# Performance work log

Hardware: AMD Instinct MI355X
Metric: run time of the kernel (lower is better)

## Reference

```python
import jax, jax.numpy as jnp
import numpy as np

N, E, H, C = 50000, 800000, 4, 64
IN_DIM = 128
HID = H * C            # 256, concat output width
VH = C // 2            # 32, value-head hidden
OUT_DIM = 4
NEG_SLOPE = 0.2
LN_EPS = 1e-5


def setup_inputs() -> dict:
    key = jax.random.key(0)
    ks = iter(jax.random.split(key, 64))
    def nrm(shape, s=0.05):
        return jax.random.normal(next(ks), shape, jnp.float32) * s
    inp = {
        "x": jax.random.normal(next(ks), (N, IN_DIM), jnp.float32),
        "edge_src": jax.random.randint(next(ks), (E,), 0, N, dtype=jnp.int32),
        "edge_dst": jax.random.randint(next(ks), (E,), 0, N, dtype=jnp.int32),
        "proj_w": nrm((C, IN_DIM)),
        "proj_b": jnp.zeros((C,), jnp.float32),
    }
    in_dims = [C, HID, HID]
    out_feats = [HID, HID, C]
    for i in range(3):
        inp[f"w{i}"] = nrm((HID, in_dims[i]))
        inp[f"asrc{i}"] = nrm((H, C))
        inp[f"adst{i}"] = nrm((H, C))
        inp[f"b{i}"] = jnp.zeros((out_feats[i],), jnp.float32)
        inp[f"g{i}"] = jnp.ones((out_feats[i],), jnp.float32)
        inp[f"be{i}"] = jnp.zeros((out_feats[i],), jnp.float32)
    inp["vw1"] = nrm((VH, C)); inp["vb1"] = jnp.zeros((VH,), jnp.float32)
    inp["vw2"] = nrm((OUT_DIM, VH)); inp["vb2"] = jnp.zeros((OUT_DIM,), jnp.float32)
    return inp


def _layer_norm(x, g, b):
    mu = x.mean(-1, keepdims=True)
    var = ((x - mu) ** 2).mean(-1, keepdims=True)
    return (x - mu) * jax.lax.rsqrt(var + LN_EPS) * g + b


def _gat_conv(x, src, dst, w, a_s, a_d, bias, concat):
    # x: [N, in_dim] -> h: [N, H, C]
    n = x.shape[0]
    h = (x @ w.T).reshape(n, H, C)
    asrc = jnp.einsum('nhc,hc->nh', h, a_s)  # [N, H]
    adst = jnp.einsum('nhc,hc->nh', h, a_d)
    # PyG default add_self_loops=True
    loop = jnp.arange(n, dtype=src.dtype)
    src_f = jnp.concatenate([src, loop])
    dst_f = jnp.concatenate([dst, loop])
    alpha = jax.nn.leaky_relu(asrc[src_f] + adst[dst_f], NEG_SLOPE)  # [E+N, H]
    # segment softmax over incoming edges of each destination node
    amax = jax.ops.segment_max(alpha, dst_f, num_segments=n)
    ex = jnp.exp(alpha - amax[dst_f])
    denom = jax.ops.segment_sum(ex, dst_f, num_segments=n)
    coef = ex / (denom[dst_f] + 1e-16)
    out = jax.ops.segment_sum(h[src_f] * coef[:, :, None], dst_f, num_segments=n)
    out = out.reshape(n, H * C) if concat else out.mean(axis=1)
    return out + bias


def _gat_layer(x, src, dst, w, a_s, a_d, bias, g, be, concat):
    # GATConv -> LayerNorm -> ELU (dropout is identity in eval)
    return jax.nn.elu(_layer_norm(_gat_conv(x, src, dst, w, a_s, a_d, bias, concat), g, be))


def reference(x, edge_src, edge_dst, proj_w, proj_b,
              w0, asrc0, adst0, b0, g0, be0,
              w1, asrc1, adst1, b1, g1, be1,
              w2, asrc2, adst2, b2, g2, be2,
              vw1, vb1, vw2, vb2):
    h = jax.nn.elu(x @ proj_w.T + proj_b)
    h = _gat_layer(h, edge_src, edge_dst, w0, asrc0, adst0, b0, g0, be0, True)
    h = _gat_layer(h, edge_src, edge_dst, w1, asrc1, adst1, b1, g1, be1, True)
    h = _gat_layer(h, edge_src, edge_dst, w2, asrc2, adst2, b2, g2, be2, False)
    v = jax.nn.elu(h @ vw1.T + vb1)
    return v @ vw2.T + vb2
```

## Files before the change

kernel.cpp:

```cpp
#include <hip/hip_runtime.h>

typedef unsigned short u16;
typedef u16 u16x4 __attribute__((ext_vector_type(4)));
typedef short short8 __attribute__((ext_vector_type(8)));
typedef float f32x4 __attribute__((ext_vector_type(4)));

__device__ __forceinline__ float elu_f(float x) { return x > 0.f ? x : expm1f(x); }
__device__ __forceinline__ float lrelu_f(float x) { return x > 0.f ? x : 0.2f * x; }

__device__ __forceinline__ u16 f2b(float f) {
  union { float f; unsigned u; } v; v.f = f;
  unsigned r = v.u + 0x7FFF + ((v.u >> 16) & 1);
  return (u16)(r >> 16);
}
__device__ __forceinline__ float b2f(u16 u) {
  union { unsigned u; float f; } v; v.u = ((unsigned)u) << 16; return v.f;
}

__global__ __launch_bounds__(256) void cvtdeg_k(const float* __restrict__ x, u16* __restrict__ xb,
                                                int nx8,
                                                const float* __restrict__ pw,
                                                const float* __restrict__ w0,
                                                const float* __restrict__ w1,
                                                const float* __restrict__ w2,
                                                u16* __restrict__ dp, u16* __restrict__ d0,
                                                u16* __restrict__ d1, u16* __restrict__ d2,
                                                const int* __restrict__ edst,
                                                int E, int n, int* __restrict__ deg) {
  int i = blockIdx.x * 256 + threadIdx.x;
  if (i < nx8) {
    int j = i * 8;
    float4 a = *reinterpret_cast<const float4*>(&x[j]);
    float4 b = *reinterpret_cast<const float4*>(&x[j + 4]);
    u16x4 o0, o1;
    o0.x = f2b(a.x); o0.y = f2b(a.y); o0.z = f2b(a.z); o0.w = f2b(a.w);
    o1.x = f2b(b.x); o1.y = f2b(b.y); o1.z = f2b(b.z); o1.w = f2b(b.w);
    *reinterpret_cast<u16x4*>(&xb[j]) = o0;
    *reinterpret_cast<u16x4*>(&xb[j + 4]) = o1;
  } else if (i < nx8 + 155648) {
    int j = i - nx8;
    if (j < 8192) dp[j] = f2b(pw[j]);
    else if (j < 24576) d0[j - 8192] = f2b(w0[j - 8192]);
    else if (j < 90112) d1[j - 24576] = f2b(w1[j - 24576]);
    else d2[j - 90112] = f2b(w2[j - 90112]);
  } else {
    int j = i - (nx8 + 155648);
    if (j < E) atomicAdd(&deg[edst[j]], 1);
    else if (j < E + n) atomicAdd(&deg[j - E], 1);
  }
}

__global__ __launch_bounds__(256) void block_sum_k(const int* __restrict__ deg,
                                                   int* __restrict__ bsum, int n) {
  int i = blockIdx.x * 256 + threadIdx.x;
  int v = (i < n) ? deg[i] : 0;
#pragma unroll
  for (int off = 1; off < 64; off <<= 1) v += __shfl_xor(v, off);
  __shared__ int ws[4];
  if ((threadIdx.x & 63) == 0) ws[threadIdx.x >> 6] = v;
  __syncthreads();
  if (threadIdx.x == 0) bsum[blockIdx.x] = ws[0] + ws[1] + ws[2] + ws[3];
}

__global__ void scan_bsum_k(int* __restrict__ bsum, int nb) {
  __shared__ int s[1024];
  int tid = threadIdx.x;
  int v = (tid < nb) ? bsum[tid] : 0;
  s[tid] = v;
  __syncthreads();
  for (int off = 1; off < 1024; off <<= 1) {
    int t = (tid >= off) ? s[tid - off] : 0;
    __syncthreads();
    s[tid] += t;
    __syncthreads();
  }
  if (tid < nb) bsum[tid] = s[tid] - v;
}

__global__ __launch_bounds__(256) void block_scan_k(const int* __restrict__ deg,
                                                    const int* __restrict__ bsum,
                                                    int* __restrict__ rowptr,
                                                    int* __restrict__ cursor, int n) {
  int i = blockIdx.x * 256 + threadIdx.x;
  int lane = threadIdx.x & 63, w = threadIdx.x >> 6;
  int v = (i < n) ? deg[i] : 0;
  int x = v;
#pragma unroll
  for (int off = 1; off < 64; off <<= 1) {
    int t = __shfl_up(x, off);
    if (lane >= off) x += t;
  }
  __shared__ int ws[4];
  if (lane == 63) ws[w] = x;
  __syncthreads();
  int add = bsum[blockIdx.x];
  for (int j = 0; j < w; ++j) add += ws[j];
  int excl = x - v + add;
  if (i < n) {
    cursor[i] = excl;
    rowptr[i + 1] = excl + v;
  }
  if (i == 0) rowptr[0] = 0;
}

__global__ __launch_bounds__(256) void scatter4_k(const int* __restrict__ src,
                                                  const int* __restrict__ dst,
                                                  int E, int EE, int* __restrict__ cursor,
                                                  int* __restrict__ col, int* __restrict__ dst2) {
  int base = (blockIdx.x * 256 + threadIdx.x) * 4;
  int s[4], d[4], pos[4];
#pragma unroll
  for (int k = 0; k < 4; ++k) {
    int e = base + k;
    if (e < E) { s[k] = src[e]; d[k] = dst[e]; }
    else if (e < EE) { s[k] = d[k] = e - E; }
    else { d[k] = -1; s[k] = 0; }
  }
#pragma unroll
  for (int k = 0; k < 4; ++k)
    if (d[k] >= 0) pos[k] = atomicAdd(&cursor[d[k]], 1);
#pragma unroll
  for (int k = 0; k < 4; ++k)
    if (d[k] >= 0) { col[pos[k]] = s[k]; dst2[pos[k]] = d[k]; }
}

template <int PROJ>
__global__ __launch_bounds__(512) void gemm2_k(const u16* __restrict__ A, int lda,
                                               const u16* __restrict__ W,
                                               const u16* __restrict__ pw,
                                               const float* __restrict__ pb,
                                               u16* __restrict__ Cb,
                                               int n, int K,
                                               const float* __restrict__ a_sv,
                                               const float* __restrict__ a_dv,
                                               float* __restrict__ asrcN,
                                               float* __restrict__ adstN) {
  __shared__ char Asb[128 * 128];
  __shared__ char Bsb[256 * 128];
  __shared__ char Xsb[PROJ ? 128 * 272 : 16];
  __shared__ char Psb[PROJ ? 64 * 272 : 16];
  const int t = threadIdx.x;
  const int lane = t & 63, w = t >> 6;
  const int wrow = w >> 2, wcol = w & 3;
  const int row0 = blockIdx.x * 128;

  if (PROJ) {
#pragma unroll
    for (int i = 0; i < 4; ++i) {
      int ci = i * 512 + t;
      int r = ci >> 4;
      int b = (ci & 15) << 4;
      int ar = row0 + r; ar = ar < n ? ar : n - 1;
      *reinterpret_cast<int4*>(Xsb + r * 272 + b) =
          *reinterpret_cast<const int4*>(&A[(size_t)ar * 128 + (b >> 1)]);
    }
#pragma unroll
    for (int i = 0; i < 2; ++i) {
      int ci = i * 512 + t;
      int r = ci >> 4;
      int b = (ci & 15) << 4;
      *reinterpret_cast<int4*>(Psb + r * 272 + b) =
          *reinterpret_cast<const int4*>(&pw[r * 128 + (b >> 1)]);
    }
    __syncthreads();
    f32x4 pacc[4];
#pragma unroll
    for (int nf = 0; nf < 4; ++nf) pacc[nf] = (f32x4){0.f, 0.f, 0.f, 0.f};
#pragma unroll
    for (int ks = 0; ks < 4; ++ks) {
      short8 paf = *reinterpret_cast<const short8*>(
          Xsb + (w * 16 + (lane & 15)) * 272 + ks * 64 + (lane >> 4) * 16);
#pragma unroll
      for (int nf = 0; nf < 4; ++nf) {
        short8 pbf = *reinterpret_cast<const short8*>(
            Psb + (nf * 16 + (lane & 15)) * 272 + ks * 64 + (lane >> 4) * 16);
        pacc[nf] = __builtin_amdgcn_mfma_f32_16x16x32_bf16(paf, pbf, pacc[nf], 0, 0, 0);
      }
    }
#pragma unroll
    for (int nf = 0; nf < 4; ++nf) {
#pragma unroll
      for (int j = 0; j < 4; ++j) {
        int rl = w * 16 + (lane >> 4) * 4 + j;
        int cg = nf * 16 + (lane & 15);
        u16 bv = f2b(elu_f(pacc[nf][j] + pb[cg]));
        *reinterpret_cast<u16*>(Asb + rl * 128 + ((cg * 2) ^ ((rl & 7) << 4))) = bv;
      }
    }
  }

  f32x4 acc[4][4];
#pragma unroll
  for (int m = 0; m < 4; ++m)
#pragma unroll
    for (int nf = 0; nf < 4; ++nf) acc[m][nf] = (f32x4){0.f, 0.f, 0.f, 0.f};

  for (int k0 = 0; k0 < K; k0 += 64) {
    if (!PROJ) {
#pragma unroll
      for (int i = 0; i < 2; ++i) {
        int ci = i * 512 + t;
        int r = ci >> 3;
        int b = (ci & 7) << 4;
        int sw = b ^ ((r & 7) << 4);
        int ar = row0 + r; ar = ar < n ? ar : n - 1;
        int4 av = *reinterpret_cast<const int4*>(&A[(size_t)ar * lda + k0 + (b >> 1)]);
        *reinterpret_cast<int4*>(Asb + r * 128 + sw) = av;
      }
    }
#pragma unroll
    for (int i = 0; i < 4; ++i) {
      int ci = i * 512 + t;
      int r = ci >> 3;
      int b = (ci & 7) << 4;
      int sw = b ^ ((r & 7) << 4);
      int4 wv = *reinterpret_cast<const int4*>(&W[(size_t)r * K + k0 + (b >> 1)]);
      *reinterpret_cast<int4*>(Bsb + r * 128 + sw) = wv;
    }
    __syncthreads();
#pragma unroll
    for (int ks = 0; ks < 2; ++ks) {
      short8 af[4], bf[4];
      int kb = ks * 64 + ((lane >> 4) << 4);
#pragma unroll
      for (int m = 0; m < 4; ++m) {
        int r = wrow * 64 + m * 16 + (lane & 15);
        af[m] = *reinterpret_cast<const short8*>(Asb + r * 128 + (kb ^ ((r & 7) << 4)));
      }
#pragma unroll
      for (int nf = 0; nf < 4; ++nf) {
        int r = wcol * 64 + nf * 16 + (lane & 15);
        bf[nf] = *reinterpret_cast<const short8*>(Bsb + r * 128 + (kb ^ ((r & 7) << 4)));
      }
#pragma unroll
      for (int m = 0; m < 4; ++m)
#pragma unroll
        for (int nf = 0; nf < 4; ++nf)
          acc[m][nf] = __builtin_amdgcn_mfma_f32_16x16x32_bf16(af[m], bf[nf], acc[m][nf], 0, 0, 0);
    }
    __syncthreads();
  }
#pragma unroll
  for (int m = 0; m < 4; ++m) {
#pragma unroll
    for (int j = 0; j < 4; ++j) {
      int rg = row0 + wrow * 64 + m * 16 + (lane >> 4) * 4 + j;
      if (rg >= n) continue;
#pragma unroll
      for (int nf = 0; nf < 4; ++nf) {
        int cg = wcol * 64 + nf * 16 + (lane & 15);
        Cb[(size_t)rg * 256 + cg] = f2b(acc[m][nf][j]);
      }
    }
  }
  {
    int h = wcol;
    int ch = lane & 15;
    float as_c[4], ad_c[4];
#pragma unroll
    for (int nf = 0; nf < 4; ++nf) {
      as_c[nf] = a_sv[h * 64 + nf * 16 + ch];
      ad_c[nf] = a_dv[h * 64 + nf * 16 + ch];
    }
#pragma unroll
    for (int m = 0; m < 4; ++m) {
#pragma unroll
      for (int j = 0; j < 4; ++j) {
        float ps = 0.f, pd = 0.f;
#pragma unroll
        for (int nf = 0; nf < 4; ++nf) {
          float v = acc[m][nf][j];
          ps += v * as_c[nf];
          pd += v * ad_c[nf];
        }
#pragma unroll
        for (int off = 1; off < 16; off <<= 1) {
          ps += __shfl_xor(ps, off);
          pd += __shfl_xor(pd, off);
        }
        int rg = row0 + wrow * 64 + m * 16 + (lane >> 4) * 4 + j;
        if ((lane & 15) == 0 && rg < n) {
          asrcN[(size_t)rg * 4 + h] = ps;
          adstN[(size_t)rg * 4 + h] = pd;
        }
      }
    }
  }
}

__global__ __launch_bounds__(256) void edge_ex2_k(const int* __restrict__ col,
                                                  const int* __restrict__ dst2,
                                                  const float* __restrict__ asrcN,
                                                  const float* __restrict__ adstN,
                                                  float* __restrict__ exT, int eep, int EE) {
  int e = blockIdx.x * 256 + threadIdx.x;
  if (e >= EE) return;
  int s = col[e], d = dst2[e];
  float4 as = *reinterpret_cast<const float4*>(&asrcN[(size_t)s * 4]);
  float4 ad = *reinterpret_cast<const float4*>(&adstN[(size_t)d * 4]);
  exT[e]            = __expf(lrelu_f(as.x + ad.x));
  exT[eep + e]      = __expf(lrelu_f(as.y + ad.y));
  exT[2 * eep + e]  = __expf(lrelu_f(as.z + ad.z));
  exT[3 * eep + e]  = __expf(lrelu_f(as.w + ad.w));
}

template <int MODE>
__global__ __launch_bounds__(256) void gat_agg4_k(const u16* __restrict__ feat,
                                                  const float* __restrict__ exT, int eep,
                                                  const int* __restrict__ rowptr,
                                                  const int* __restrict__ col,
                                                  const float* __restrict__ bias,
                                                  const float* __restrict__ g,
                                                  const float* __restrict__ be,
                                                  void* __restrict__ out, int n) {
  int wave = threadIdx.x >> 6, lane = threadIdx.x & 63;
  int node = blockIdx.x * 4 + wave;
  if (node >= n) return;
  int h = lane >> 4;
  const float* exh = exT + (size_t)h * eep;
  int s0 = rowptr[node], s1 = rowptr[node + 1];
  float ax = 0.f, ay = 0.f, az = 0.f, aw = 0.f, den = 0.f;
  int e = s0;
  for (; e + 8 <= s1; e += 8) {
    int p0 = col[e + 0], p1 = col[e + 1], p2 = col[e + 2], p3 = col[e + 3];
    int q0 = col[e + 4], q1 = col[e + 5], q2 = col[e + 6], q3 = col[e + 7];
    float u0 = exh[e + 0], u1 = exh[e + 1], u2 = exh[e + 2], u3 = exh[e + 3];
    float v0 = exh[e + 4], v1 = exh[e + 5], v2 = exh[e + 6], v3 = exh[e + 7];
    u16x4 fp0 = *reinterpret_cast<const u16x4*>(&feat[(size_t)p0 * 256 + lane * 4]);
    u16x4 fp1 = *reinterpret_cast<const u16x4*>(&feat[(size_t)p1 * 256 + lane * 4]);
    u16x4 fp2 = *reinterpret_cast<const u16x4*>(&feat[(size_t)p2 * 256 + lane * 4]);
    u16x4 fp3 = *reinterpret_cast<const u16x4*>(&feat[(size_t)p3 * 256 + lane * 4]);
    u16x4 fq0 = *reinterpret_cast<const u16x4*>(&feat[(size_t)q0 * 256 + lane * 4]);
    u16x4 fq1 = *reinterpret_cast<const u16x4*>(&feat[(size_t)q1 * 256 + lane * 4]);
    u16x4 fq2 = *reinterpret_cast<const u16x4*>(&feat[(size_t)q2 * 256 + lane * 4]);
    u16x4 fq3 = *reinterpret_cast<const u16x4*>(&feat[(size_t)q3 * 256 + lane * 4]);
    den += ((u0 + u1) + (u2 + u3)) + ((v0 + v1) + (v2 + v3));
    ax += u0 * b2f(fp0.x) + u1 * b2f(fp1.x) + u2 * b2f(fp2.x) + u3 * b2f(fp3.x);
    ay += u0 * b2f(fp0.y) + u1 * b2f(fp1.y) + u2 * b2f(fp2.y) + u3 * b2f(fp3.y);
    az += u0 * b2f(fp0.z) + u1 * b2f(fp1.z) + u2 * b2f(fp2.z) + u3 * b2f(fp3.z);
    aw += u0 * b2f(fp0.w) + u1 * b2f(fp1.w) + u2 * b2f(fp2.w) + u3 * b2f(fp3.w);
    ax += v0 * b2f(fq0.x) + v1 * b2f(fq1.x) + v2 * b2f(fq2.x) + v3 * b2f(fq3.x);
    ay += v0 * b2f(fq0.y) + v1 * b2f(fq1.y) + v2 * b2f(fq2.y) + v3 * b2f(fq3.y);
    az += v0 * b2f(fq0.z) + v1 * b2f(fq1.z) + v2 * b2f(fq2.z) + v3 * b2f(fq3.z);
    aw += v0 * b2f(fq0.w) + v1 * b2f(fq1.w) + v2 * b2f(fq2.w) + v3 * b2f(fq3.w);
  }
  for (; e + 4 <= s1; e += 4) {
    int p0 = col[e + 0], p1 = col[e + 1], p2 = col[e + 2], p3 = col[e + 3];
    float u0 = exh[e + 0], u1 = exh[e + 1], u2 = exh[e + 2], u3 = exh[e + 3];
    u16x4 fp0 = *reinterpret_cast<const u16x4*>(&feat[(size_t)p0 * 256 + lane * 4]);
    u16x4 fp1 = *reinterpret_cast<const u16x4*>(&feat[(size_t)p1 * 256 + lane * 4]);
    u16x4 fp2 = *reinterpret_cast<const u16x4*>(&feat[(size_t)p2 * 256 + lane * 4]);
    u16x4 fp3 = *reinterpret_cast<const u16x4*>(&feat[(size_t)p3 * 256 + lane * 4]);
    den += (u0 + u1) + (u2 + u3);
    ax += u0 * b2f(fp0.x) + u1 * b2f(fp1.x) + u2 * b2f(fp2.x) + u3 * b2f(fp3.x);
    ay += u0 * b2f(fp0.y) + u1 * b2f(fp1.y) + u2 * b2f(fp2.y) + u3 * b2f(fp3.y);
    az += u0 * b2f(fp0.z) + u1 * b2f(fp1.z) + u2 * b2f(fp2.z) + u3 * b2f(fp3.z);
    aw += u0 * b2f(fp0.w) + u1 * b2f(fp1.w) + u2 * b2f(fp2.w) + u3 * b2f(fp3.w);
  }
  for (; e < s1; ++e) {
    int s = col[e];
    float xv = exh[e];
    den += xv;
    u16x4 f = *reinterpret_cast<const u16x4*>(&feat[(size_t)s * 256 + lane * 4]);
    ax += xv * b2f(f.x); ay += xv * b2f(f.y); az += xv * b2f(f.z); aw += xv * b2f(f.w);
  }
  float inv = 1.f / den;
  ax *= inv; ay *= inv; az *= inv; aw *= inv;

  if (MODE == 0) {
    float4 b4 = *reinterpret_cast<const float4*>(&bias[lane * 4]);
    float vx = ax + b4.x, vy = ay + b4.y, vz = az + b4.z, vw = aw + b4.w;
    float s = vx + vy + vz + vw;
#pragma unroll
    for (int off = 1; off < 64; off <<= 1) s += __shfl_xor(s, off);
    float mu = s * (1.f / 256.f);
    float dx = vx - mu, dy = vy - mu, dz = vz - mu, dw = vw - mu;
    float q = dx * dx + dy * dy + dz * dz + dw * dw;
#pragma unroll
    for (int off = 1; off < 64; off <<= 1) q += __shfl_xor(q, off);
    float inv2 = rsqrtf(q * (1.f / 256.f) + 1e-5f);
    float4 gg = *reinterpret_cast<const float4*>(&g[lane * 4]);
    float4 bb = *reinterpret_cast<const float4*>(&be[lane * 4]);
    u16x4 o;
    o.x = f2b(elu_f(dx * inv2 * gg.x + bb.x));
    o.y = f2b(elu_f(dy * inv2 * gg.y + bb.y));
    o.z = f2b(elu_f(dz * inv2 * gg.z + bb.z));
    o.w = f2b(elu_f(dw * inv2 * gg.w + bb.w));
    u16* rowb = (u16*)out + (size_t)node * 256;
    *reinterpret_cast<u16x4*>(&rowb[lane * 4]) = o;
  } else {
    ax += __shfl_xor(ax, 16); ax += __shfl_xor(ax, 32);
    ay += __shfl_xor(ay, 16); ay += __shfl_xor(ay, 32);
    az += __shfl_xor(az, 16); az += __shfl_xor(az, 32);
    aw += __shfl_xor(aw, 16); aw += __shfl_xor(aw, 32);
    int qd = lane & 15;
    float4 b4 = *reinterpret_cast<const float4*>(&bias[qd * 4]);
    float vx = 0.25f * ax + b4.x, vy = 0.25f * ay + b4.y;
    float vz = 0.25f * az + b4.z, vw = 0.25f * aw + b4.w;
    float s = vx + vy + vz + vw;
#pragma unroll
    for (int off = 1; off < 64; off <<= 1) s += __shfl_xor(s, off);
    float mu = s * (1.f / 256.f);
    float dx = vx - mu, dy = vy - mu, dz = vz - mu, dw = vw - mu;
    float q = dx * dx + dy * dy + dz * dz + dw * dw;
#pragma unroll
    for (int off = 1; off < 64; off <<= 1) q += __shfl_xor(q, off);
    float inv2 = rsqrtf(q * (1.f / 256.f) + 1e-5f);
    if (lane < 16) {
      float4 gg = *reinterpret_cast<const float4*>(&g[qd * 4]);
      float4 bb = *reinterpret_cast<const float4*>(&be[qd * 4]);
      float4 o;
      o.x = elu_f(dx * inv2 * gg.x + bb.x);
      o.y = elu_f(dy * inv2 * gg.y + bb.y);
      o.z = elu_f(dz * inv2 * gg.z + bb.z);
      o.w = elu_f(dw * inv2 * gg.w + bb.w);
      *reinterpret_cast<float4*>(&((float*)out)[(size_t)node * 64 + qd * 4]) = o;
    }
  }
}

__global__ __launch_bounds__(256) void value_head_k(const float* __restrict__ hh,
                                                    const float* __restrict__ vw1,
                                                    const float* __restrict__ vb1,
                                                    const float* __restrict__ vw2,
                                                    const float* __restrict__ vb2,
                                                    float* __restrict__ out, int n) {
  __shared__ float w1s[32 * 65];
  __shared__ float hs[4][64];
  __shared__ float vs[4][33];
  int tid = threadIdx.x;
  for (int i = tid; i < 2048; i += 256) w1s[(i >> 6) * 65 + (i & 63)] = vw1[i];
  int wave = tid >> 6, lane = tid & 63;
  int node = blockIdx.x * 4 + wave;
  int nc = node < n ? node : n - 1;
  hs[wave][lane] = hh[(size_t)nc * 64 + lane];
  __syncthreads();
  int j = lane & 31, half = lane >> 5;
  float p = 0.f;
#pragma unroll
  for (int c = 0; c < 32; ++c) p += hs[wave][half * 32 + c] * w1s[j * 65 + half * 32 + c];
  p += __shfl_xor(p, 32);
  float v = elu_f(p + vb1[j]);
  if (half == 0) vs[wave][j] = v;
  __syncthreads();
  if (lane < 4 && node < n) {
    float o = vb2[lane];
#pragma unroll
    for (int jj = 0; jj < 32; ++jj) o += vs[wave][jj] * vw2[lane * 32 + jj];
    out[(size_t)node * 4 + lane] = o;
  }
}

extern "C" void kernel_launch(void* const* d_in, const int* in_sizes, int n_in,
                              void* d_out, int out_size, void* d_ws, size_t ws_size,
                              hipStream_t stream) {
  const float* x      = (const float*)d_in[0];
  const int*   esrc   = (const int*)d_in[1];
  const int*   edst   = (const int*)d_in[2];
  const float* proj_w = (const float*)d_in[3];
  const float* proj_b = (const float*)d_in[4];
  const float* w[3]   = {(const float*)d_in[5],  (const float*)d_in[11], (const float*)d_in[17]};
  const float* a_s[3] = {(const float*)d_in[6],  (const float*)d_in[12], (const float*)d_in[18]};
  const float* a_d[3] = {(const float*)d_in[7],  (const float*)d_in[13], (const float*)d_in[19]};
  const float* bb[3]  = {(const float*)d_in[8],  (const float*)d_in[14], (const float*)d_in[20]};
  const float* gg[3]  = {(const float*)d_in[9],  (const float*)d_in[15], (const float*)d_in[21]};
  const float* be[3]  = {(const float*)d_in[10], (const float*)d_in[16], (const float*)d_in[22]};
  const float* vw1 = (const float*)d_in[23];
  const float* vb1 = (const float*)d_in[24];
  const float* vw2 = (const float*)d_in[25];
  const float* vb2 = (const float*)d_in[26];
  float* outp = (float*)d_out;

  const int n = in_sizes[0] / 128;
  const int E = in_sizes[1];
  const int EE = E + n;
  const int eep = (EE + 255) & ~255;
  const int nbl = (n + 255) / 256;

  char* p = (char*)d_ws;
  auto alloc = [&](size_t bytes) { char* r = p; p += (bytes + 255) & ~(size_t)255; return r; };
  u16*   hA    = (u16*)alloc((size_t)n * 512);
  u16*   featB = (u16*)alloc((size_t)n * 512);
  u16*   xb    = (u16*)alloc((size_t)n * 256);
  float* exT   = (float*)alloc((size_t)eep * 16);
  float* asrcN = (float*)alloc((size_t)n * 16);
  float* adstN = (float*)alloc((size_t)n * 16);
  u16* wbp = (u16*)alloc(64 * 128 * 2);
  u16* wb[3];
  wb[0] = (u16*)alloc(256 * 64 * 2);
  wb[1] = (u16*)alloc(256 * 256 * 2);
  wb[2] = (u16*)alloc(256 * 256 * 2);
  int* deg    = (int*)alloc((size_t)n * 4);
  int* rowptr = (int*)alloc((size_t)(n + 1) * 4);
  int* cursor = (int*)alloc((size_t)n * 4);
  int* col    = (int*)alloc((size_t)EE * 4);
  int* dst2   = (int*)alloc((size_t)EE * 4);
  int* bsum   = (int*)alloc((size_t)nbl * 4);
  float* hfinal = (float*)hA;

  hipMemsetAsync(deg, 0, (size_t)n * sizeof(int), stream);
  const int nx8 = n * 16;
  cvtdeg_k<<<(nx8 + 155648 + EE + 255) / 256, 256, 0, stream>>>(
      x, xb, nx8, proj_w, w[0], w[1], w[2], wbp, wb[0], wb[1], wb[2], edst, E, n, deg);
  block_sum_k<<<nbl, 256, 0, stream>>>(deg, bsum, n);
  scan_bsum_k<<<1, 1024, 0, stream>>>(bsum, nbl);
  block_scan_k<<<nbl, 256, 0, stream>>>(deg, bsum, rowptr, cursor, n);
  scatter4_k<<<(EE + 1023) / 1024, 256, 0, stream>>>(esrc, edst, E, EE, cursor, col, dst2);

  const int nb4 = (n + 3) / 4;
  const int nbg = (n + 127) / 128;
  dim3 blk(256);

  const int Kin[3] = {64, 256, 256};
  for (int i = 0; i < 3; ++i) {
    if (i == 0) {
      gemm2_k<1><<<nbg, 512, 0, stream>>>(xb, 128, wb[0], wbp, proj_b, featB,
                                          n, 64, a_s[0], a_d[0], asrcN, adstN);
    } else {
      gemm2_k<0><<<nbg, 512, 0, stream>>>(hA, 256, wb[i], nullptr, nullptr, featB,
                                          n, Kin[i], a_s[i], a_d[i], asrcN, adstN);
    }
    edge_ex2_k<<<(EE + 255) / 256, 256, 0, stream>>>(col, dst2, asrcN, adstN, exT, eep, EE);
    if (i < 2) {
      gat_agg4_k<0><<<nb4, blk, 0, stream>>>(featB, exT, eep, rowptr, col, bb[i], gg[i], be[i],
                                             (void*)hA, n);
    } else {
      gat_agg4_k<1><<<nb4, blk, 0, stream>>>(featB, exT, eep, rowptr, col, bb[i], gg[i], be[i],
                                             (void*)hfinal, n);
    }
  }

  value_head_k<<<nb4, blk, 0, stream>>>(hfinal, vw1, vb1, vw2, vb2, outp, n);
}
```

Baseline: 415.7 us.

## Record atomic ranks during degree count and pack CSR col/dst into int2

The degree-count atomics now also store each edge's rank within its destination. The scatter pass then computes the CSR position as rowptr[d]+rank[e] with no second round of atomics, and the cursor array is dropped. col and dst2 are merged into one int2 array, so edge_ex2 reads 8 contiguous bytes per edge. The cost is an extra rank buffer, and the aggregation kernel now reads strided int2 entries where it only needs the col half, which doubles the bytes it pulls for indices.

```diff
diff --git a/kernel.cpp b/kernel.cpp
--- a/kernel.cpp
+++ b/kernel.cpp
@@ -26,7 +26,8 @@
                                                 u16* __restrict__ dp, u16* __restrict__ d0,
                                                 u16* __restrict__ d1, u16* __restrict__ d2,
                                                 const int* __restrict__ edst,
-                                                int E, int n, int* __restrict__ deg) {
+                                                int E, int EE, int* __restrict__ deg,
+                                                int* __restrict__ rank) {
   int i = blockIdx.x * 256 + threadIdx.x;
   if (i < nx8) {
     int j = i * 8;
@@ -45,8 +46,8 @@
     else d2[j - 90112] = f2b(w2[j - 90112]);
   } else {
     int j = i - (nx8 + 155648);
-    if (j < E) atomicAdd(&deg[edst[j]], 1);
-    else if (j < E + n) atomicAdd(&deg[j - E], 1);
+    if (j < E) rank[j] = atomicAdd(&deg[edst[j]], 1);
+    else if (j < EE) rank[j] = atomicAdd(&deg[j - E], 1);
   }
 }
 
@@ -79,8 +80,7 @@
 
 __global__ __launch_bounds__(256) void block_scan_k(const int* __restrict__ deg,
                                                     const int* __restrict__ bsum,
-                                                    int* __restrict__ rowptr,
-                                                    int* __restrict__ cursor, int n) {
+                                                    int* __restrict__ rowptr, int n) {
   int i = blockIdx.x * 256 + threadIdx.x;
   int lane = threadIdx.x & 63, w = threadIdx.x >> 6;
   int v = (i < n) ? deg[i] : 0;
@@ -96,32 +96,27 @@
   int add = bsum[blockIdx.x];
   for (int j = 0; j < w; ++j) add += ws[j];
   int excl = x - v + add;
-  if (i < n) {
-    cursor[i] = excl;
-    rowptr[i + 1] = excl + v;
-  }
+  if (i < n) rowptr[i + 1] = excl + v;
   if (i == 0) rowptr[0] = 0;
 }
 
-__global__ __launch_bounds__(256) void scatter4_k(const int* __restrict__ src,
+__global__ __launch_bounds__(256) void scatterf_k(const int* __restrict__ src,
                                                   const int* __restrict__ dst,
-                                                  int E, int EE, int* __restrict__ cursor,
-                                                  int* __restrict__ col, int* __restrict__ dst2) {
+                                                  const int* __restrict__ rank,
+                                                  const int* __restrict__ rowptr,
+                                                  int E, int EE, int2* __restrict__ colpk) {
   int base = (blockIdx.x * 256 + threadIdx.x) * 4;
-  int s[4], d[4], pos[4];
 #pragma unroll
   for (int k = 0; k < 4; ++k) {
     int e = base + k;
-    if (e < E) { s[k] = src[e]; d[k] = dst[e]; }
-    else if (e < EE) { s[k] = d[k] = e - E; }
-    else { d[k] = -1; s[k] = 0; }
-  }
-#pragma unroll
-  for (int k = 0; k < 4; ++k)
-    if (d[k] >= 0) pos[k] = atomicAdd(&cursor[d[k]], 1);
-#pragma unroll
-  for (int k = 0; k < 4; ++k)
-    if (d[k] >= 0) { col[pos[k]] = s[k]; dst2[pos[k]] = d[k]; }
+    if (e < EE) {
+      int s, d;
+      if (e < E) { s = src[e]; d = dst[e]; }
+      else { s = d = e - E; }
+      int pos = rowptr[d] + rank[e];
+      colpk[pos] = make_int2(s, d);
+    }
+  }
 }
 
 template <int PROJ>
@@ -288,16 +283,15 @@
   }
 }
 
-__global__ __launch_bounds__(256) void edge_ex2_k(const int* __restrict__ col,
-                                                  const int* __restrict__ dst2,
+__global__ __launch_bounds__(256) void edge_ex2_k(const int2* __restrict__ colpk,
                                                   const float* __restrict__ asrcN,
                                                   const float* __restrict__ adstN,
                                                   float* __restrict__ exT, int eep, int EE) {
   int e = blockIdx.x * 256 + threadIdx.x;
   if (e >= EE) return;
-  int s = col[e], d = dst2[e];
-  float4 as = *reinterpret_cast<const float4*>(&asrcN[(size_t)s * 4]);
-  float4 ad = *reinterpret_cast<const float4*>(&adstN[(size_t)d * 4]);
+  int2 cd = colpk[e];
+  float4 as = *reinterpret_cast<const float4*>(&asrcN[(size_t)cd.x * 4]);
+  float4 ad = *reinterpret_cast<const float4*>(&adstN[(size_t)cd.y * 4]);
   exT[e]            = __expf(lrelu_f(as.x + ad.x));
   exT[eep + e]      = __expf(lrelu_f(as.y + ad.y));
   exT[2 * eep + e]  = __expf(lrelu_f(as.z + ad.z));
@@ -308,7 +302,7 @@
 __global__ __launch_bounds__(256) void gat_agg4_k(const u16* __restrict__ feat,
                                                   const float* __restrict__ exT, int eep,
                                                   const int* __restrict__ rowptr,
-                                                  const int* __restrict__ col,
+                                                  const int2* __restrict__ colpk,
                                                   const float* __restrict__ bias,
                                                   const float* __restrict__ g,
                                                   const float* __restrict__ be,
@@ -322,8 +316,8 @@
   float ax = 0.f, ay = 0.f, az = 0.f, aw = 0.f, den = 0.f;
   int e = s0;
   for (; e + 8 <= s1; e += 8) {
-    int p0 = col[e + 0], p1 = col[e + 1], p2 = col[e + 2], p3 = col[e + 3];
-    int q0 = col[e + 4], q1 = col[e + 5], q2 = col[e + 6], q3 = col[e + 7];
+    int p0 = colpk[e + 0].x, p1 = colpk[e + 1].x, p2 = colpk[e + 2].x, p3 = colpk[e + 3].x;
+    int q0 = colpk[e + 4].x, q1 = colpk[e + 5].x, q2 = colpk[e + 6].x, q3 = colpk[e + 7].x;
     float u0 = exh[e + 0], u1 = exh[e + 1], u2 = exh[e + 2], u3 = exh[e + 3];
     float v0 = exh[e + 4], v1 = exh[e + 5], v2 = exh[e + 6], v3 = exh[e + 7];
     u16x4 fp0 = *reinterpret_cast<const u16x4*>(&feat[(size_t)p0 * 256 + lane * 4]);
@@ -345,7 +339,7 @@
     aw += v0 * b2f(fq0.w) + v1 * b2f(fq1.w) + v2 * b2f(fq2.w) + v3 * b2f(fq3.w);
   }
   for (; e + 4 <= s1; e += 4) {
-    int p0 = col[e + 0], p1 = col[e + 1], p2 = col[e + 2], p3 = col[e + 3];
+    int p0 = colpk[e + 0].x, p1 = colpk[e + 1].x, p2 = colpk[e + 2].x, p3 = colpk[e + 3].x;
     float u0 = exh[e + 0], u1 = exh[e + 1], u2 = exh[e + 2], u3 = exh[e + 3];
     u16x4 fp0 = *reinterpret_cast<const u16x4*>(&feat[(size_t)p0 * 256 + lane * 4]);
     u16x4 fp1 = *reinterpret_cast<const u16x4*>(&feat[(size_t)p1 * 256 + lane * 4]);
@@ -358,7 +352,7 @@
     aw += u0 * b2f(fp0.w) + u1 * b2f(fp1.w) + u2 * b2f(fp2.w) + u3 * b2f(fp3.w);
   }
   for (; e < s1; ++e) {
-    int s = col[e];
+    int s = colpk[e].x;
     float xv = exh[e];
     den += xv;
     u16x4 f = *reinterpret_cast<const u16x4*>(&feat[(size_t)s * 256 + lane * 4]);
@@ -492,20 +486,19 @@
   wb[2] = (u16*)alloc(256 * 256 * 2);
   int* deg    = (int*)alloc((size_t)n * 4);
   int* rowptr = (int*)alloc((size_t)(n + 1) * 4);
-  int* cursor = (int*)alloc((size_t)n * 4);
-  int* col    = (int*)alloc((size_t)EE * 4);
-  int* dst2   = (int*)alloc((size_t)EE * 4);
+  int* rank   = (int*)alloc((size_t)EE * 4);
+  int2* colpk = (int2*)alloc((size_t)EE * 8);
   int* bsum   = (int*)alloc((size_t)nbl * 4);
   float* hfinal = (float*)hA;
 
   hipMemsetAsync(deg, 0, (size_t)n * sizeof(int), stream);
   const int nx8 = n * 16;
   cvtdeg_k<<<(nx8 + 155648 + EE + 255) / 256, 256, 0, stream>>>(
-      x, xb, nx8, proj_w, w[0], w[1], w[2], wbp, wb[0], wb[1], wb[2], edst, E, n, deg);
+      x, xb, nx8, proj_w, w[0], w[1], w[2], wbp, wb[0], wb[1], wb[2], edst, E, EE, deg, rank);
   block_sum_k<<<nbl, 256, 0, stream>>>(deg, bsum, n);
   scan_bsum_k<<<1, 1024, 0, stream>>>(bsum, nbl);
-  block_scan_k<<<nbl, 256, 0, stream>>>(deg, bsum, rowptr, cursor, n);
-  scatter4_k<<<(EE + 1023) / 1024, 256, 0, stream>>>(esrc, edst, E, EE, cursor, col, dst2);
+  block_scan_k<<<nbl, 256, 0, stream>>>(deg, bsum, rowptr, n);
+  scatterf_k<<<(EE + 1023) / 1024, 256, 0, stream>>>(esrc, edst, rank, rowptr, E, EE, colpk);
 
   const int nb4 = (n + 3) / 4;
   const int nbg = (n + 127) / 128;
@@ -520,12 +513,12 @@
       gemm2_k<0><<<nbg, 512, 0, stream>>>(hA, 256, wb[i], nullptr, nullptr, featB,
                                           n, Kin[i], a_s[i], a_d[i], asrcN, adstN);
     }
-    edge_ex2_k<<<(EE + 255) / 256, 256, 0, stream>>>(col, dst2, asrcN, adstN, exT, eep, EE);
+    edge_ex2_k<<<(EE + 255) / 256, 256, 0, stream>>>(colpk, asrcN, adstN, exT, eep, EE);
     if (i < 2) {
-      gat_agg4_k<0><<<nb4, blk, 0, stream>>>(featB, exT, eep, rowptr, col, bb[i], gg[i], be[i],
+      gat_agg4_k<0><<<nb4, blk, 0, stream>>>(featB, exT, eep, rowptr, colpk, bb[i], gg[i], be[i],
                                              (void*)hA, n);
     } else {
-      gat_agg4_k<1><<<nb4, blk, 0, stream>>>(featB, exT, eep, rowptr, col, bb[i], gg[i], be[i],
+      gat_agg4_k<1><<<nb4, blk, 0, stream>>>(featB, exT, eep, rowptr, colpk, bb[i], gg[i], be[i],
                                              (void*)hfinal, n);
     }
   }
```

After: 385.8 us. -7.2%, faster.
